# Performance work log

Hardware: AMD Instinct MI355X
Metric: run time of the kernel (lower is better)

## Reference

```python
import jax, jax.numpy as jnp
import numpy as np

LAMBDA_W = 1.0
NEG_INF = -1e10


def setup_inputs() -> dict:
    key = jax.random.key(0)
    k1, k2, k3 = jax.random.split(key, 3)
    B, L, D = 8, 2048, 256
    h_x = jax.random.normal(k1, (B, L, D), dtype=jnp.float32)
    h_y = jax.random.normal(k2, (B, L, D), dtype=jnp.float32)
    # masks: valid prefix of 3/4 length, padded tail of zeros (exercises masking)
    valid = (3 * L) // 4
    base = (jnp.arange(L) < valid).astype(jnp.float32)
    x_mask = jnp.broadcast_to(base, (B, L))
    y_mask = jnp.broadcast_to(base, (B, L))
    # biaffine weight (n_label=1, no biases), init_value scaling kept at O(1)
    W = jax.random.normal(k3, (D, D), dtype=jnp.float32) / jnp.sqrt(jnp.float32(D))
    return {"h_x": h_x, "h_y": h_y, "x_mask": x_mask, "y_mask": y_mask, "W": W}


def reference(h_x, h_y, x_mask, y_mask, W):
    # src = h_x [B,Ls,D], pred = h_y [B,Lp,D]
    src, pred = h_x, h_y
    src_mask, pred_mask = x_mask, y_mask

    # cost_mx[b,p,s] = ||src[b,s] - pred[b,p]||_2, via ||a||^2+||b||^2-2ab
    src_sq = jnp.sum(src * src, axis=-1)            # [B,Ls]
    pred_sq = jnp.sum(pred * pred, axis=-1)         # [B,Lp]
    cross = jnp.einsum('bpd,bsd->bps', pred, src)   # [B,Lp,Ls]
    cost_mx = jnp.sqrt(jnp.maximum(pred_sq[:, :, None] + src_sq[:, None, :] - 2.0 * cross, 0.0))

    # biaffine scores: pred W src^T  -> [B,Lp,Ls]
    tr_mx = jnp.einsum('bpd,de,bse->bps', pred, W, src)

    # cost_mask[b,p,s] = pred_mask[b,p]*src_mask[b,s]
    cost_mask = pred_mask[:, :, None] * src_mask[:, None, :]
    tr_mx = jnp.where(cost_mask == 0, NEG_INF, tr_mx)
    tr_prob = jax.nn.softmax(tr_mx, axis=-1)

    flow_cost = tr_prob * cost_mx                   # [B,Lp,Ls]

    nL1 = jnp.sum(pred_mask, axis=-1, keepdims=True)  # [B,1]
    nL2 = jnp.sum(src_mask, axis=-1, keepdims=True)   # [B,1]
    fc = jnp.sum(flow_cost, axis=(1, 2), keepdims=True)  # [B,1,1]
    fc = fc / (nL1 * nL2)   # broadcasts [B,1,1]/[B,1] -> [B,B,1], matches torch
    fc = jnp.mean(fc)
    return fc * LAMBDA_W
```

## Files before the change

kernel.cpp:

```cpp
#include <hip/hip_runtime.h>
#include <math.h>
#include <stdint.h>

#define B_ 8
#define L_ 2048
#define D_ 256
#define NEG_INF_V (-1e10f)
#define NSTRIP 32

typedef __bf16 bf16x8 __attribute__((ext_vector_type(8)));
typedef float f32x4 __attribute__((ext_vector_type(4)));

#define MFMA16(a, b, c) __builtin_amdgcn_mfma_f32_16x16x32_bf16((a), (b), (c), 0, 0, 0)


__global__ __launch_bounds__(256) void convert_kernel(
    const float* __restrict__ x, const float* __restrict__ y,
    const float* __restrict__ W,
    __bf16* __restrict__ srcFM, __bf16* __restrict__ predFM,
    __bf16* __restrict__ WFM,
    float* __restrict__ src_sq, float* __restrict__ pred_sq) {
    int tid = threadIdx.x;
    int blk = blockIdx.x;
    if (blk < 2048) {
        const float* in = (blk < 1024) ? x : y;
        __bf16* out = (blk < 1024) ? srcFM : predFM;
        float* sqout = (blk < 1024) ? src_sq : pred_sq;
        int g = blk & 1023;
        __shared__ __align__(16) __bf16 sFM[512 * 8];
        __shared__ float sSQ[16];
        int kb = (tid & 31) >> 2, qq = tid & 3;
        #pragma unroll
        for (int pass = 0; pass < 2; ++pass) {
            int m = pass * 8 + (tid >> 5);
            const float* p = in + ((size_t)g * 16 + m) * D_ + (tid & 31) * 8;
            float4 v0 = *(const float4*)p;
            float4 v1 = *(const float4*)(p + 4);
            float ss = v0.x * v0.x + v0.y * v0.y + v0.z * v0.z + v0.w * v0.w +
                       v1.x * v1.x + v1.y * v1.y + v1.z * v1.z + v1.w * v1.w;
            #pragma unroll
            for (int o = 16; o > 0; o >>= 1) ss += __shfl_xor(ss, o, 64);
            if ((tid & 31) == 0) sSQ[m] = ss;
            union { __bf16 o[8]; bf16x8 v; } cv;
            cv.o[0] = (__bf16)v0.x; cv.o[1] = (__bf16)v0.y;
            cv.o[2] = (__bf16)v0.z; cv.o[3] = (__bf16)v0.w;
            cv.o[4] = (__bf16)v1.x; cv.o[5] = (__bf16)v1.y;
            cv.o[6] = (__bf16)v1.z; cv.o[7] = (__bf16)v1.w;
            *(bf16x8*)(sFM + (m * 32 + kb * 4 + qq) * 8) = cv.v;
        }
        __syncthreads();
        int G0 = tid * 2;
        int kb0 = G0 >> 6, q0 = (G0 >> 4) & 3, m0 = G0 & 15;
        bf16x8 a = *(const bf16x8*)(sFM + (m0 * 32 + kb0 * 4 + q0) * 8);
        bf16x8 bgr = *(const bf16x8*)(sFM + ((m0 + 1) * 32 + kb0 * 4 + q0) * 8);
        *(bf16x8*)(out + ((size_t)g * 512 + G0) * 8) = a;
        *(bf16x8*)(out + ((size_t)g * 512 + G0 + 1) * 8) = bgr;
        if (tid < 16) sqout[g * 16 + tid] = sSQ[tid];
    } else {
        int idx = (blk - 2048) * 256 + tid;
        int m = idx & 15, q = (idx >> 4) & 3, kb = (idx >> 6) & 7, gn = idx >> 9;
        union { __bf16 o[8]; bf16x8 v; } cv;
        #pragma unroll
        for (int j = 0; j < 8; ++j)
            cv.o[j] = (__bf16)W[(size_t)(kb * 32 + q * 8 + j) * D_ + gn * 16 + m];
        *(bf16x8*)(WFM + (size_t)idx * 8) = cv.v;
    }
}

__global__ __launch_bounds__(256, 2) void predw_mfma(
    const __bf16* __restrict__ predFM, const __bf16* __restrict__ WFM,
    const float* __restrict__ pred_mask, __bf16* __restrict__ pwFM) {
    __shared__ __align__(16) __bf16 sT[128 * 136];
    __shared__ int flag;
    int tid = threadIdx.x, lane = tid & 63, wid = tid >> 6;
    int wp = wid >> 1, wn = wid & 1;
    int id = blockIdx.x;
    int m0 = (((id >> 3) & 15) + (id & 7) * 16) * 128;
    int n0 = (id >> 7) * 128;
    if (tid == 0) flag = 0;
    __syncthreads();
    if (tid < 128) { if (pred_mask[m0 + tid] != 0.f) atomicOr(&flag, 1); }
    __syncthreads();
    if (!flag) return;

    const __bf16* bA = predFM + (size_t)(m0 / 16 + wp * 4) * 4096 + lane * 8;
    const __bf16* bB = WFM + (size_t)(n0 / 16 + wn * 4) * 4096 + lane * 8;
    f32x4 acc[4][4] = {};
    #pragma unroll
    for (int kb = 0; kb < 8; ++kb) {
        bf16x8 fA[4], fB[4];
        #pragma unroll
        for (int t = 0; t < 4; ++t) {
            fA[t] = *(const bf16x8*)(bA + (t * 8 + kb) * 512);
            fB[t] = *(const bf16x8*)(bB + (t * 8 + kb) * 512);
        }
        #pragma unroll
        for (int pt = 0; pt < 4; ++pt)
            #pragma unroll
            for (int st = 0; st < 4; ++st)
                acc[pt][st] = MFMA16(fA[pt], fB[st], acc[pt][st]);
    }
    int q = lane >> 4, cn = lane & 15;
    #pragma unroll
    for (int pt = 0; pt < 4; ++pt)
        #pragma unroll
        for (int st = 0; st < 4; ++st)
            #pragma unroll
            for (int r = 0; r < 4; ++r)
                sT[(wp * 64 + pt * 16 + q * 4 + r) * 136 + wn * 64 + st * 16 + cn] =
                    (__bf16)acc[pt][st][r];
    __syncthreads();
    #pragma unroll
    for (int i = 0; i < 8; ++i) {
        int idx = i * 256 + tid;
        int gl = idx >> 8, kbl = (idx >> 6) & 3, qq = (idx >> 4) & 3, mm = idx & 15;
        bf16x8 v = *(const bf16x8*)(sT + (gl * 16 + mm) * 136 + kbl * 32 + qq * 8);
        *(bf16x8*)(pwFM +
                   (((size_t)(m0 / 16 + gl) * 8 + n0 / 32 + kbl) * 64 + qq * 16 + mm) * 8) = v;
    }
}

__global__ __launch_bounds__(256, 6) void fused_mfma(
    const __bf16* __restrict__ srcFM, const __bf16* __restrict__ predFM,
    const __bf16* __restrict__ pwFM,
    const float* __restrict__ src_mask, const float* __restrict__ pred_mask,
    const float* __restrict__ src_sq, const float* __restrict__ pred_sq,
    float* __restrict__ m_part, float* __restrict__ l_part,
    float* __restrict__ w_part, float* __restrict__ Sarr,
    unsigned int* __restrict__ counter) {
    __shared__ float sPM[64], sPSQ[64], sSM[64], sSSQ[64];
    __shared__ int flg[4];
    int tid = threadIdx.x, lane = tid & 63, wid = tid >> 6;
    int id = blockIdx.x;
    int b = id & 7, px = (id >> 3) & 31, sy = id >> 8;
    int p0 = px * 64;

    if (id == 0) {
        if (tid == 0) *counter = 0u;
        if (tid < 24) Sarr[tid] = 0.f;
    }
    if (tid < 4) flg[tid] = 0;
    __syncthreads();
    if (tid < 64) {
        float v = pred_mask[b * L_ + p0 + tid];
        sPM[tid] = v;
        sPSQ[tid] = pred_sq[b * L_ + p0 + tid];
        atomicOr(&flg[(v != 0.f) ? 0 : 1], 1);
    } else if (tid < 128) {
        int t = tid - 64;
        float v = src_mask[b * L_ + sy * 64 + t];
        sSM[t] = v;
        sSSQ[t] = src_sq[b * L_ + sy * 64 + t];
        atomicOr(&flg[(v != 0.f) ? 2 : 3], 1);
    }
    __syncthreads();
    const bool anyVP = flg[0] != 0, anyIP = flg[1] != 0, anyVS = flg[2] != 0;
    const bool doT = anyVP && anyVS;
    const bool doG = anyVS || anyIP;
    if (!doG) {
        if (tid < 64) {
            size_t o = (size_t)sy * (B_ * L_) + b * L_ + p0 + tid;
            m_part[o] = NEG_INF_V; l_part[o] = 64.f; w_part[o] = 0.f;
        }
        return;
    }

    const __bf16* bS = srcFM + ((size_t)(b * 128 + sy * 4)) * 4096 + lane * 8;
    const __bf16* bP = predFM + ((size_t)(b * 128 + px * 4 + wid)) * 4096 + lane * 8;
    const __bf16* bW = pwFM + ((size_t)(b * 128 + px * 4 + wid)) * 4096 + lane * 8;

    f32x4 aT[4] = {};
    f32x4 aG[4] = {};
    if (doT) {
        #pragma unroll
        for (int kb = 0; kb < 8; ++kb) {
            bf16x8 fP = *(const bf16x8*)(bP + kb * 512);
            bf16x8 fW = *(const bf16x8*)(bW + kb * 512);
            bf16x8 fB[4];
            #pragma unroll
            for (int t = 0; t < 4; ++t)
                fB[t] = *(const bf16x8*)(bS + (t * 8 + kb) * 512);
            #pragma unroll
            for (int t = 0; t < 4; ++t) {
                aG[t] = MFMA16(fP, fB[t], aG[t]);
                aT[t] = MFMA16(fW, fB[t], aT[t]);
            }
        }
    } else {
        #pragma unroll
        for (int kb = 0; kb < 8; ++kb) {
            bf16x8 fP = *(const bf16x8*)(bP + kb * 512);
            bf16x8 fB[4];
            #pragma unroll
            for (int t = 0; t < 4; ++t)
                fB[t] = *(const bf16x8*)(bS + (t * 8 + kb) * 512);
            #pragma unroll
            for (int t = 0; t < 4; ++t)
                aG[t] = MFMA16(fP, fB[t], aG[t]);
        }
    }

    int q = lane >> 4, cn = lane & 15;
    float smv[4], sqv[4];
    #pragma unroll
    for (int t = 0; t < 4; ++t) {
        smv[t] = sSM[t * 16 + cn];
        sqv[t] = sSSQ[t * 16 + cn];
    }
    int rbase = wid * 16 + q * 4;
    #pragma unroll
    for (int r = 0; r < 4; ++r) {
        float pm = sPM[rbase + r], psq = sPSQ[rbase + r];
        float tv[4], cst[4];
        float tm = -1e30f;
        #pragma unroll
        for (int t = 0; t < 4; ++t) {
            cst[t] = __builtin_amdgcn_sqrtf(
                fmaxf(psq + sqv[t] - 2.f * aG[t][r], 0.f));
            float tt = doT ? aT[t][r] : NEG_INF_V;
            tv[t] = (pm == 0.f) ? 0.f : (smv[t] != 0.f ? tt : NEG_INF_V);
            tm = fmaxf(tm, tv[t]);
        }
        #pragma unroll
        for (int o = 8; o > 0; o >>= 1) tm = fmaxf(tm, __shfl_xor(tm, o, 16));
        float l = 0.f, w = 0.f;
        #pragma unroll
        for (int t = 0; t < 4; ++t) {
            float e = __expf(tv[t] - tm);
            l += e;
            w = fmaf(e, cst[t], w);
        }
        #pragma unroll
        for (int o = 8; o > 0; o >>= 1) {
            l += __shfl_xor(l, o, 16);
            w += __shfl_xor(w, o, 16);
        }
        if (cn == 0) {
            size_t o = (size_t)sy * (B_ * L_) + b * L_ + p0 + rbase + r;
            m_part[o] = tm;
            l_part[o] = l;
            w_part[o] = w;
        }
    }
}

__global__ __launch_bounds__(256) void combine_kernel(
    const float* __restrict__ m_part, const float* __restrict__ l_part,
    const float* __restrict__ w_part,
    const float* __restrict__ x_mask, const float* __restrict__ y_mask,
    float* __restrict__ Sarr, unsigned int* __restrict__ counter,
    float* __restrict__ out) {
    int tid = threadIdx.x;
    int r = blockIdx.x * 256 + tid;
    int b = r >> 11;
    float mm = -1e30f;
    #pragma unroll
    for (int s = 0; s < NSTRIP; ++s) mm = fmaxf(mm, m_part[(size_t)s * (B_ * L_) + r]);
    float l = 0.f, w = 0.f;
    #pragma unroll
    for (int s = 0; s < NSTRIP; ++s) {
        size_t o = (size_t)s * (B_ * L_) + r;
        float e = __expf(m_part[o] - mm);
        l = fmaf(l_part[o], e, l);
        w = fmaf(w_part[o], e, w);
    }
    float sv = w / l;
    float n1 = y_mask[r], n2 = x_mask[r];
    __shared__ float red[3][256];
    red[0][tid] = sv; red[1][tid] = n1; red[2][tid] = n2;
    __syncthreads();
    for (int o = 128; o > 0; o >>= 1) {
        if (tid < o) {
            red[0][tid] += red[0][tid + o];
            red[1][tid] += red[1][tid + o];
            red[2][tid] += red[2][tid + o];
        }
        __syncthreads();
    }
    __shared__ int isLast;
    if (tid == 0) {
        atomicAdd(&Sarr[b], red[0][0]);
        atomicAdd(&Sarr[8 + b], red[1][0]);
        atomicAdd(&Sarr[16 + b], red[2][0]);
        __threadfence();
        isLast = (atomicAdd(counter, 1u) == 63u) ? 1 : 0;
    }
    __syncthreads();
    if (isLast) {
        __shared__ float fb[24];
        if (tid < 24) fb[tid] = atomicAdd(&Sarr[tid], 0.f);
        __syncthreads();
        if (tid == 0) {
            float ss = 0.f, si = 0.f;
            for (int bb = 0; bb < B_; bb++) {
                ss += fb[bb];
                si += 1.0f / (fb[8 + bb] * fb[16 + bb]);
            }
            out[0] = ss * si / (float)(B_ * B_);
        }
    }
}

extern "C" void kernel_launch(void* const* d_in, const int* in_sizes, int n_in,
                              void* d_out, int out_size, void* d_ws, size_t ws_size,
                              hipStream_t stream) {
    const float* h_x = (const float*)d_in[0];
    const float* h_y = (const float*)d_in[1];
    const float* x_mask = (const float*)d_in[2];
    const float* y_mask = (const float*)d_in[3];
    const float* W = (const float*)d_in[4];

    char* w8 = (char*)d_ws;
    const size_t BLD2 = (size_t)B_ * L_ * D_ * 2;
    __bf16* srcFM = (__bf16*)w8;
    __bf16* predFM = (__bf16*)(w8 + BLD2);
    __bf16* pwFM = (__bf16*)(w8 + 2 * BLD2);
    __bf16* WFM = (__bf16*)(w8 + 3 * BLD2);
    float* src_sq = (float*)(w8 + 3 * BLD2 + (1 << 17));
    float* pred_sq = (float*)(w8 + 3 * BLD2 + (1 << 17) + (1 << 16));
    char* pbase = w8 + 3 * BLD2 + (1 << 17) + (1 << 17);
    const size_t PSZ = (size_t)B_ * L_ * NSTRIP * 4;
    float* m_part = (float*)pbase;
    float* l_part = (float*)(pbase + PSZ);
    float* w_part = (float*)(pbase + 2 * PSZ);
    float* Sarr = (float*)(pbase + 3 * PSZ);
    unsigned int* counter = (unsigned int*)(pbase + 3 * PSZ + 128);

    convert_kernel<<<2080, 256, 0, stream>>>(h_x, h_y, W, srcFM, predFM, WFM,
                                             src_sq, pred_sq);
    predw_mfma<<<256, 256, 0, stream>>>(predFM, WFM, y_mask, pwFM);
    fused_mfma<<<8192, 256, 0, stream>>>(
        srcFM, predFM, pwFM, x_mask, y_mask, src_sq, pred_sq,
        m_part, l_part, w_part, Sarr, counter);
    combine_kernel<<<B_ * L_ / 256, 256, 0, stream>>>(
        m_part, l_part, w_part, x_mask, y_mask, Sarr, counter, (float*)d_out);
}
```

Baseline: 141.5 us.

## Enlarge fused tile to 128x128 with src strip staged in LDS

The fused kernel now runs 512-thread blocks, each covering 128 pred rows by 128 src columns instead of 64x64. The src strip (64 KB of bf16) is staged in shared memory and shared by all eight waves, and each wave computes two 16-row pred tiles, so pred, predW and src operands are reused more and global traffic drops. In exchange, the 64 KB of LDS per block and larger register footprint limit occupancy to a few blocks per CU. The mask-skip decisions become coarser because they are now made per 128x128 tile.

```diff
diff --git a/kernel.cpp b/kernel.cpp
--- a/kernel.cpp
+++ b/kernel.cpp
@@ -120,7 +120,7 @@
     }
 }
 
-__global__ __launch_bounds__(256, 6) void fused_mfma(
+__global__ __launch_bounds__(512, 4) void fused_mfma(
     const __bf16* __restrict__ srcFM, const __bf16* __restrict__ predFM,
     const __bf16* __restrict__ pwFM,
     const float* __restrict__ src_mask, const float* __restrict__ pred_mask,
@@ -128,12 +128,14 @@
     float* __restrict__ m_part, float* __restrict__ l_part,
     float* __restrict__ w_part, float* __restrict__ Sarr,
     unsigned int* __restrict__ counter) {
-    __shared__ float sPM[64], sPSQ[64], sSM[64], sSSQ[64];
+    __shared__ __align__(16) __bf16 sS[128 * 256];
+    __shared__ float sPM[128], sPSQ[128], sSM[128], sSSQ[128];
     __shared__ int flg[4];
     int tid = threadIdx.x, lane = tid & 63, wid = tid >> 6;
+    int wp = wid >> 1, ws = wid & 1;
     int id = blockIdx.x;
-    int b = id & 7, px = (id >> 3) & 31, sy = id >> 8;
-    int p0 = px * 64;
+    int b = id & 7, px = (id >> 3) & 15, syb = id >> 7;
+    int p0 = px * 128, s0 = syb * 128;
 
     if (id == 0) {
         if (tid == 0) *counter = 0u;
@@ -141,62 +143,80 @@
     }
     if (tid < 4) flg[tid] = 0;
     __syncthreads();
-    if (tid < 64) {
+    if (tid < 128) {
         float v = pred_mask[b * L_ + p0 + tid];
         sPM[tid] = v;
         sPSQ[tid] = pred_sq[b * L_ + p0 + tid];
         atomicOr(&flg[(v != 0.f) ? 0 : 1], 1);
-    } else if (tid < 128) {
-        int t = tid - 64;
-        float v = src_mask[b * L_ + sy * 64 + t];
+    } else if (tid < 256) {
+        int t = tid - 128;
+        float v = src_mask[b * L_ + s0 + t];
         sSM[t] = v;
-        sSSQ[t] = src_sq[b * L_ + sy * 64 + t];
+        sSSQ[t] = src_sq[b * L_ + s0 + t];
         atomicOr(&flg[(v != 0.f) ? 2 : 3], 1);
+    }
+    {
+        const __bf16* g = srcFM + ((size_t)(b * 128 + syb * 8)) * 4096;
+        #pragma unroll
+        for (int i = 0; i < 8; ++i) {
+            size_t off = (size_t)i * 4096 + tid * 8;
+            *(bf16x8*)(sS + off) = *(const bf16x8*)(g + off);
+        }
     }
     __syncthreads();
     const bool anyVP = flg[0] != 0, anyIP = flg[1] != 0, anyVS = flg[2] != 0;
     const bool doT = anyVP && anyVS;
     const bool doG = anyVS || anyIP;
     if (!doG) {
-        if (tid < 64) {
-            size_t o = (size_t)sy * (B_ * L_) + b * L_ + p0 + tid;
+        if (tid < 256) {
+            int half = tid >> 7, t = tid & 127;
+            size_t o = (size_t)(syb * 2 + half) * (B_ * L_) + b * L_ + p0 + t;
             m_part[o] = NEG_INF_V; l_part[o] = 64.f; w_part[o] = 0.f;
         }
         return;
     }
 
-    const __bf16* bS = srcFM + ((size_t)(b * 128 + sy * 4)) * 4096 + lane * 8;
-    const __bf16* bP = predFM + ((size_t)(b * 128 + px * 4 + wid)) * 4096 + lane * 8;
-    const __bf16* bW = pwFM + ((size_t)(b * 128 + px * 4 + wid)) * 4096 + lane * 8;
-
-    f32x4 aT[4] = {};
-    f32x4 aG[4] = {};
+    const __bf16* bP = predFM + ((size_t)(b * 128 + px * 8 + wp * 2)) * 4096 + lane * 8;
+    const __bf16* bW = pwFM + ((size_t)(b * 128 + px * 8 + wp * 2)) * 4096 + lane * 8;
+    const __bf16* bS = sS + (size_t)(ws * 4) * 4096 + lane * 8;
+
+    f32x4 aG[2][4] = {};
+    f32x4 aT[2][4] = {};
     if (doT) {
         #pragma unroll
         for (int kb = 0; kb < 8; ++kb) {
-            bf16x8 fP = *(const bf16x8*)(bP + kb * 512);
-            bf16x8 fW = *(const bf16x8*)(bW + kb * 512);
-            bf16x8 fB[4];
+            bf16x8 fP[2], fW[2], fB[4];
+            #pragma unroll
+            for (int m = 0; m < 2; ++m) {
+                fP[m] = *(const bf16x8*)(bP + (m * 8 + kb) * 512);
+                fW[m] = *(const bf16x8*)(bW + (m * 8 + kb) * 512);
+            }
             #pragma unroll
             for (int t = 0; t < 4; ++t)
                 fB[t] = *(const bf16x8*)(bS + (t * 8 + kb) * 512);
             #pragma unroll
-            for (int t = 0; t < 4; ++t) {
-                aG[t] = MFMA16(fP, fB[t], aG[t]);
-                aT[t] = MFMA16(fW, fB[t], aT[t]);
-            }
+            for (int m = 0; m < 2; ++m)
+                #pragma unroll
+                for (int t = 0; t < 4; ++t) {
+                    aG[m][t] = MFMA16(fP[m], fB[t], aG[m][t]);
+                    aT[m][t] = MFMA16(fW[m], fB[t], aT[m][t]);
+                }
         }
     } else {
         #pragma unroll
         for (int kb = 0; kb < 8; ++kb) {
-            bf16x8 fP = *(const bf16x8*)(bP + kb * 512);
-            bf16x8 fB[4];
+            bf16x8 fP[2], fB[4];
+            #pragma unroll
+            for (int m = 0; m < 2; ++m)
+                fP[m] = *(const bf16x8*)(bP + (m * 8 + kb) * 512);
             #pragma unroll
             for (int t = 0; t < 4; ++t)
                 fB[t] = *(const bf16x8*)(bS + (t * 8 + kb) * 512);
             #pragma unroll
-            for (int t = 0; t < 4; ++t)
-                aG[t] = MFMA16(fP, fB[t], aG[t]);
+            for (int m = 0; m < 2; ++m)
+                #pragma unroll
+                for (int t = 0; t < 4; ++t)
+                    aG[m][t] = MFMA16(fP[m], fB[t], aG[m][t]);
         }
     }
 
@@ -204,42 +224,46 @@
     float smv[4], sqv[4];
     #pragma unroll
     for (int t = 0; t < 4; ++t) {
-        smv[t] = sSM[t * 16 + cn];
-        sqv[t] = sSSQ[t * 16 + cn];
-    }
-    int rbase = wid * 16 + q * 4;
-    #pragma unroll
-    for (int r = 0; r < 4; ++r) {
-        float pm = sPM[rbase + r], psq = sPSQ[rbase + r];
-        float tv[4], cst[4];
-        float tm = -1e30f;
-        #pragma unroll
-        for (int t = 0; t < 4; ++t) {
-            cst[t] = __builtin_amdgcn_sqrtf(
-                fmaxf(psq + sqv[t] - 2.f * aG[t][r], 0.f));
-            float tt = doT ? aT[t][r] : NEG_INF_V;
-            tv[t] = (pm == 0.f) ? 0.f : (smv[t] != 0.f ? tt : NEG_INF_V);
-            tm = fmaxf(tm, tv[t]);
-        }
-        #pragma unroll
-        for (int o = 8; o > 0; o >>= 1) tm = fmaxf(tm, __shfl_xor(tm, o, 16));
-        float l = 0.f, w = 0.f;
-        #pragma unroll
-        for (int t = 0; t < 4; ++t) {
-            float e = __expf(tv[t] - tm);
-            l += e;
-            w = fmaf(e, cst[t], w);
-        }
-        #pragma unroll
-        for (int o = 8; o > 0; o >>= 1) {
-            l += __shfl_xor(l, o, 16);
-            w += __shfl_xor(w, o, 16);
-        }
-        if (cn == 0) {
-            size_t o = (size_t)sy * (B_ * L_) + b * L_ + p0 + rbase + r;
-            m_part[o] = tm;
-            l_part[o] = l;
-            w_part[o] = w;
+        smv[t] = sSM[ws * 64 + t * 16 + cn];
+        sqv[t] = sSSQ[ws * 64 + t * 16 + cn];
+    }
+    int syp = syb * 2 + ws;
+    #pragma unroll
+    for (int m = 0; m < 2; ++m) {
+        int rbase = wp * 32 + m * 16 + q * 4;
+        #pragma unroll
+        for (int r = 0; r < 4; ++r) {
+            float pm = sPM[rbase + r], psq = sPSQ[rbase + r];
+            float tv[4], cst[4];
+            float tm = -1e30f;
+            #pragma unroll
+            for (int t = 0; t < 4; ++t) {
+                cst[t] = __builtin_amdgcn_sqrtf(
+                    fmaxf(psq + sqv[t] - 2.f * aG[m][t][r], 0.f));
+                float tt = doT ? aT[m][t][r] : NEG_INF_V;
+                tv[t] = (pm == 0.f) ? 0.f : (smv[t] != 0.f ? tt : NEG_INF_V);
+                tm = fmaxf(tm, tv[t]);
+            }
+            #pragma unroll
+            for (int o = 8; o > 0; o >>= 1) tm = fmaxf(tm, __shfl_xor(tm, o, 16));
+            float l = 0.f, w = 0.f;
+            #pragma unroll
+            for (int t = 0; t < 4; ++t) {
+                float e = __expf(tv[t] - tm);
+                l += e;
+                w = fmaf(e, cst[t], w);
+            }
+            #pragma unroll
+            for (int o = 8; o > 0; o >>= 1) {
+                l += __shfl_xor(l, o, 16);
+                w += __shfl_xor(w, o, 16);
+            }
+            if (cn == 0) {
+                size_t o = (size_t)syp * (B_ * L_) + b * L_ + p0 + rbase + r;
+                m_part[o] = tm;
+                l_part[o] = l;
+                w_part[o] = w;
+            }
         }
     }
 }
@@ -329,7 +353,7 @@
     convert_kernel<<<2080, 256, 0, stream>>>(h_x, h_y, W, srcFM, predFM, WFM,
                                              src_sq, pred_sq);
     predw_mfma<<<256, 256, 0, stream>>>(predFM, WFM, y_mask, pwFM);
-    fused_mfma<<<8192, 256, 0, stream>>>(
+    fused_mfma<<<2048, 512, 0, stream>>>(
         srcFM, predFM, pwFM, x_mask, y_mask, src_sq, pred_sq,
         m_part, l_part, w_part, Sarr, counter);
     combine_kernel<<<B_ * L_ / 256, 256, 0, stream>>>(
```

After: 140.2 us. About the same (-0.9%).
